# Performance work log

Hardware: AMD Instinct MI355X
Metric: run time of the kernel (lower is better)

Reference implementation:

```python
import jax, jax.numpy as jnp
import numpy as np

N = 524288          # total atoms (sorted by degree)
E = 1433600         # total directed bonds
B, L = 16384, 32    # molecules x atoms-per-molecule (B*L == N)
NODE, EDGE, H, OUT = 64, 16, 128, 128
N0 = 8192           # number of degree-0 atoms
DEG_COUNTS = {1: 65536, 2: 131072, 3: 196608, 4: 98304, 5: 24576}
BN_EPS = 1e-5


def setup_inputs() -> dict:
    key = jax.random.key(0)
    ks = jax.random.split(key, 24)
    inp = {}
    inp["node_feat"] = jax.random.normal(ks[0], (N, NODE), jnp.float32)
    inp["edge_feat"] = jax.random.normal(ks[1], (E, EDGE), jnp.float32)
    i = 2
    for d in (1, 2, 3, 4, 5):
        n_d = DEG_COUNTS[d]
        inp[f"nbr_node_d{d}"] = jax.random.randint(ks[i], (n_d, d), 0, N, jnp.int32); i += 1
        inp[f"nbr_edge_d{d}"] = jax.random.randint(ks[i], (n_d, d), 0, E, jnp.int32); i += 1
    inp["atom_index"] = jnp.arange(B * L, dtype=jnp.int32).reshape(B, L)

    def lin(k, o, fan_in):
        return jax.random.normal(k, (o, fan_in), jnp.float32) / np.sqrt(fan_in).astype(np.float32)

    inp["out_W0"] = lin(ks[12], OUT, NODE); inp["out_b0"] = jnp.zeros((OUT,), jnp.float32)
    inp["out_W1"] = lin(ks[13], OUT, H);    inp["out_b1"] = jnp.zeros((OUT,), jnp.float32)
    inp["out_W2"] = lin(ks[14], OUT, H);    inp["out_b2"] = jnp.zeros((OUT,), jnp.float32)
    inp["conv0_selfW"] = lin(ks[15], H, NODE)
    inp["conv0_degW"] = jax.random.normal(ks[16], (5, H, NODE + EDGE), jnp.float32) / np.sqrt(NODE + EDGE).astype(np.float32)
    inp["conv0_bias"] = jnp.zeros((1, H), jnp.float32)
    inp["conv1_selfW"] = lin(ks[17], H, H)
    inp["conv1_degW"] = jax.random.normal(ks[18], (5, H, H + EDGE), jnp.float32) / np.sqrt(H + EDGE).astype(np.float32)
    inp["conv1_bias"] = jnp.zeros((1, H), jnp.float32)
    return inp


def _graph_degree_conv(node_repr, edge_repr, selfW, degW, bias, nbr_nodes, nbr_edges):
    out_size = selfW.shape[0]
    # degree 0: zero neighbor contribution
    parts = [jnp.zeros((N0, out_size), node_repr.dtype)]
    for di, d in enumerate((1, 2, 3, 4, 5)):
        nn_rep = node_repr[nbr_nodes[di]]          # [n_d, d, node]
        ee_rep = edge_repr[nbr_edges[di]]          # [n_d, d, edge]
        summed = jnp.concatenate([nn_rep.sum(1), ee_rep.sum(1)], axis=-1)  # [n_d, node+edge]
        parts.append(summed @ degW[di].T)          # per-degree linear (no bias)
    neighbor_repr = jnp.concatenate(parts, axis=0)  # nodes sorted by degree -> aligned
    act = node_repr @ selfW.T + neighbor_repr + bias
    # BatchNorm1d(affine=False), training-mode batch stats (biased variance)
    mean = act.mean(0)
    var = act.var(0)
    act = (act - mean) / jnp.sqrt(var + BN_EPS)
    return jax.nn.relu(act)


def reference(node_feat, edge_feat,
              nbr_node_d1, nbr_edge_d1, nbr_node_d2, nbr_edge_d2,
              nbr_node_d3, nbr_edge_d3, nbr_node_d4, nbr_edge_d4,
              nbr_node_d5, nbr_edge_d5, atom_index,
              out_W0, out_b0, out_W1, out_b1, out_W2, out_b2,
              conv0_selfW, conv0_degW, conv0_bias,
              conv1_selfW, conv1_degW, conv1_bias):
    nbr_nodes = (nbr_node_d1, nbr_node_d2, nbr_node_d3, nbr_node_d4, nbr_node_d5)
    nbr_edges = (nbr_edge_d1, nbr_edge_d2, nbr_edge_d3, nbr_edge_d4, nbr_edge_d5)

    x = node_feat
    acc = jax.nn.softmax(x @ out_W0.T + out_b0, axis=1)
    x = _graph_degree_conv(x, edge_feat, conv0_selfW, conv0_degW, conv0_bias, nbr_nodes, nbr_edges)
    acc = acc + jax.nn.softmax(x @ out_W1.T + out_b1, axis=1)
    x = _graph_degree_conv(x, edge_feat, conv1_selfW, conv1_degW, conv1_bias, nbr_nodes, nbr_edges)
    acc = acc + jax.nn.softmax(x @ out_W2.T + out_b2, axis=1)
    # scatter per-atom activations into [batch, max_len, OUT]
    return acc[atom_index]
```

## Files before the change

kernel.cpp:

```cpp
#include <hip/hip_runtime.h>
#include <hip/hip_bf16.h>
#include <math.h>


typedef short  short8   __attribute__((ext_vector_type(8)));
typedef unsigned short ushort8v __attribute__((ext_vector_type(8)));
typedef float  f32x4    __attribute__((ext_vector_type(4)));
typedef unsigned int u32;

static constexpr int  N_ATOMS = 524288;
static constexpr long NROWCOL = (long)N_ATOMS * 128;
static constexpr int  NBLK    = N_ATOMS / 64;

__device__ __forceinline__ float bf2f(ushort h) {
    return __uint_as_float(((unsigned)h) << 16);
}
__device__ __forceinline__ ushort f2bf(float x) {
    unsigned u = __float_as_uint(x);
    return (ushort)((u + 0x7fffu + ((u >> 16) & 1u)) >> 16);
}

__device__ __forceinline__ uint4 pack8(const float v[8]) {
    union { __hip_bfloat162 h2[4]; uint4 u; } c;
#pragma unroll
    for (int e = 0; e < 4; ++e)
        c.h2[e] = __float22bfloat162_rn(make_float2(v[2*e], v[2*e+1]));
    return c.u;
}
__device__ __forceinline__ short8 pack8s(const float v[8]) {
    union { uint4 u; short8 s; } c;
    c.u = pack8(v);
    return c.s;
}
__device__ __forceinline__ ushort f2bf1(float x) {
    union { __hip_bfloat16 b; ushort u; } c;
    c.b = __float2bfloat16(x);
    return c.u;
}

__device__ __forceinline__ void gload_lds16(const ushort* g, ushort* l) {
    __builtin_amdgcn_global_load_lds(
        (const __attribute__((address_space(1))) u32*)g,
        (__attribute__((address_space(3))) u32*)l, 16, 0, 0);
}

__device__ __forceinline__ void seg_of(long r, int& d, long& off) {
    if      (r < 73728)  { d = 1; off = 8192;  }
    else if (r < 204800) { d = 2; off = 73728; }
    else if (r < 401408) { d = 3; off = 204800;}
    else if (r < 499712) { d = 4; off = 401408;}
    else                 { d = 5; off = 499712;}
}

__global__ __launch_bounds__(256)
void esum_kernel(const float* __restrict__ edge_feat,
                 const int* __restrict__ ne1, const int* __restrict__ ne2,
                 const int* __restrict__ ne3, const int* __restrict__ ne4,
                 const int* __restrict__ ne5, ushort* __restrict__ esumb)
{
    const long t = (long)blockIdx.x * 256 + threadIdx.x;
    const long r = 8192 + (t >> 1);
    const int  h = (int)(t & 1);
    int d; long off; seg_of(r, d, off);
    const int* ne = (d==1)?ne1:(d==2)?ne2:(d==3)?ne3:(d==4)?ne4:ne5;
    const long i0 = (r - off) * d;
    float v[8] = {0,0,0,0,0,0,0,0};
    for (int j = 0; j < d; ++j) {
        const long e = ne[i0 + j];
        const float4* p = (const float4*)(edge_feat + e * 16 + h * 8);
        const float4 a = p[0], b = p[1];
        v[0]+=a.x; v[1]+=a.y; v[2]+=a.z; v[3]+=a.w;
        v[4]+=b.x; v[5]+=b.y; v[6]+=b.z; v[7]+=b.w;
    }
    *(uint4*)(esumb + (r - 8192) * 16 + h * 8) = pack8(v);
}

__global__ void wprep(const float* __restrict__ src, ushort* __restrict__ dst,
                      int rows, int Ks, int Kd)
{
    const int i = blockIdx.x * 256 + threadIdx.x;
    if (i >= rows * Kd) return;
    const int r = i / Kd, c = i % Kd;
    dst[i] = f2bf(c < Ks ? src[r * Ks + c] : 0.f);
}

__global__ void wprep_img(const float* __restrict__ src, ushort* __restrict__ dst, int K)
{
    const int i = blockIdx.x * 256 + threadIdx.x;
    if (i >= 128 * K) return;
    const int row = i / K, col = i % K;
    dst[(col >> 3) * 1024 + row * 8 + (col & 7)] = f2bf(src[i]);
}

template<int NG, bool F32, bool BN>
__device__ __forceinline__ void stage_rows(const void* Xv, long r0,
                                           ushort* __restrict__ Ab,
                                           const float* __restrict__ statsL)
{
    for (int t = threadIdx.x; t < 64 * NG; t += 256) {
        const int row = t / NG, g = t % NG;
        const long gr = r0 + row;
        uint4 w;
        if (F32) {
            const float4* p = (const float4*)((const float*)Xv + gr * (long)(NG * 8) + g * 8);
            const float4 a = p[0], b = p[1];
            const float v[8] = {a.x,a.y,a.z,a.w,b.x,b.y,b.z,b.w};
            w = pack8(v);
        } else if (BN) {
            const int c0 = g * 8;
            const ushort8v u = *(const ushort8v*)((const ushort*)Xv + gr * (long)(NG * 8) + g * 8);
            float v[8];
#pragma unroll
            for (int e = 0; e < 8; ++e)
                v[e] = fmaxf(fmaf(bf2f(u[e]), statsL[c0 + e], statsL[128 + c0 + e]), 0.f);
            w = pack8(v);
        } else {
            w = *(const uint4*)((const ushort*)Xv + gr * (long)(NG * 8) + g * 8);
        }
        ((uint4*)Ab)[row * NG + (g ^ (row & 7))] = w;
    }
}

template<int NGL, int NST, int NGN, bool F32, bool BN>
__device__ __forceinline__ void stage_gather(const void* Xv,
                                             const ushort* __restrict__ esumb,
                                             const int* __restrict__ nnl, int d,
                                             long r0, ushort* __restrict__ Ab,
                                             const float* __restrict__ statsL)
{
    for (int t = threadIdx.x; t < 64 * NST; t += 256) {
        const int row = t / NST, g = t % NST;
        uint4 w = {0, 0, 0, 0};
        if (g < NGN) {
            const int c0 = g * 8;
            float v[8] = {0,0,0,0,0,0,0,0};
            for (int j = 0; j < d; ++j) {
                const long idx = nnl[row * d + j];
                if (F32) {
                    const float4* p = (const float4*)((const float*)Xv + idx * (long)(NGN * 8) + c0);
                    const float4 a = p[0], b = p[1];
                    v[0]+=a.x; v[1]+=a.y; v[2]+=a.z; v[3]+=a.w;
                    v[4]+=b.x; v[5]+=b.y; v[6]+=b.z; v[7]+=b.w;
                } else {
                    const ushort8v u = *(const ushort8v*)((const ushort*)Xv + idx * (long)(NGN * 8) + c0);
#pragma unroll
                    for (int e = 0; e < 8; ++e) {
                        float x = bf2f(u[e]);
                        if (BN) x = fmaxf(fmaf(x, statsL[c0 + e], statsL[128 + c0 + e]), 0.f);
                        v[e] += x;
                    }
                }
            }
            w = pack8(v);
        } else if (g < NGN + 2) {
            const long er = r0 + row - 8192;
            w = *(const uint4*)(esumb + er * 16 + (g - NGN) * 8);
        }
        ((uint4*)Ab)[row * NGL + (g ^ (row & 7))] = w;
    }
}

template<int KS, int NG>
__device__ __forceinline__ void mfma_lds(const ushort* __restrict__ Ab,
                                         const ushort* __restrict__ Wb, int KP,
                                         int wc, f32x4 acc[4][2])
{
    const int lane = threadIdx.x & 63;
    const int lg = lane >> 4, lr = lane & 15;
#pragma unroll
    for (int ks = 0; ks < KS; ++ks) {
        short8 B0 = *(const short8*)(Wb + (long)(wc + lr) * KP + ks * 32 + 8 * lg);
        short8 B1 = *(const short8*)(Wb + (long)(wc + 16 + lr) * KP + ks * 32 + 8 * lg);
        const int gk = ks * 4 + lg;
#pragma unroll
        for (int m = 0; m < 4; ++m) {
            const int row = 16 * m + lr;
            const short8 a = *(const short8*)(Ab + (row * NG + (gk ^ (row & 7))) * 8);
            acc[m][0] = __builtin_amdgcn_mfma_f32_16x16x32_bf16(a, B0, acc[m][0], 0, 0, 0);
            acc[m][1] = __builtin_amdgcn_mfma_f32_16x16x32_bf16(a, B1, acc[m][1], 0, 0, 0);
        }
    }
}

template<int K1, bool A1F32, bool BNIN, int NGL2, int NST2, int NGN2, int KS2, int KP2>
__global__ __launch_bounds__(256, 2)
void conv_kernel(const void* __restrict__ X, const ushort* __restrict__ Wb1,
                 const ushort* __restrict__ Wb2base,
                 const int* __restrict__ nn1, const int* __restrict__ nn2,
                 const int* __restrict__ nn3, const int* __restrict__ nn4,
                 const int* __restrict__ nn5,
                 const ushort* __restrict__ esumb, const float* __restrict__ cbias,
                 const float* __restrict__ stats_in,
                 ushort* __restrict__ act_out, float* __restrict__ part)
{
    constexpr int NG1 = K1 / 8;
    constexpr int KS1 = K1 / 32;
    constexpr int NGMAX = (NGL2 > NG1) ? NGL2 : NG1;
    __shared__ uint4 AbV[64 * NGMAX];
    __shared__ int   nnl[320];
    __shared__ float statsL[256];
    ushort* Ab = (ushort*)AbV;

    const long r0 = (long)blockIdx.x * 64;
    const int wid = threadIdx.x >> 6, lane = threadIdx.x & 63;
    const int lg = lane >> 4, lr = lane & 15, wc = wid * 32;

    if (BNIN)
        for (int t = threadIdx.x; t < 256; t += 256) statsL[t] = stats_in[t];

    int d = 0;
    const bool has2 = (r0 >= 8192);
    if (has2) {
        long off; seg_of(r0, d, off);
        const int* nn = (d==1)?nn1:(d==2)?nn2:(d==3)?nn3:(d==4)?nn4:nn5;
        const long i0 = (r0 - off) * d;
        for (int t = threadIdx.x; t < 64 * d; t += 256) nnl[t] = nn[i0 + t];
    }
    __syncthreads();

    stage_rows<NG1, A1F32, BNIN>(X, r0, Ab, statsL);
    __syncthreads();
    f32x4 acc[4][2] = {};
    mfma_lds<KS1, NG1>(Ab, Wb1, K1, wc, acc);

    if (has2) {
        __syncthreads();
        stage_gather<NGL2, NST2, NGN2, A1F32, BNIN>(X, esumb, nnl, d, r0, Ab, statsL);
        __syncthreads();
        const ushort* Wb2 = Wb2base + (long)(d - 1) * 128 * KP2;
        mfma_lds<KS2, NGL2>(Ab, Wb2, KP2, wc, acc);
    }

#pragma unroll
    for (int n = 0; n < 2; ++n) {
        const float bv = cbias[wc + n * 16 + lr];
#pragma unroll
        for (int m = 0; m < 4; ++m)
#pragma unroll
            for (int j = 0; j < 4; ++j) acc[m][n][j] += bv;
    }
#pragma unroll
    for (int m = 0; m < 4; ++m)
#pragma unroll
        for (int j = 0; j < 4; ++j) {
            const long row = r0 + 16 * m + 4 * lg + j;
#pragma unroll
            for (int n = 0; n < 2; ++n)
                act_out[row * 128 + wc + n * 16 + lr] = f2bf1(acc[m][n][j]);
        }
#pragma unroll
    for (int n = 0; n < 2; ++n) {
        float s = 0.f, q = 0.f;
#pragma unroll
        for (int m = 0; m < 4; ++m)
#pragma unroll
            for (int j = 0; j < 4; ++j) { const float v = acc[m][n][j]; s += v; q += v * v; }
        s += __shfl_xor(s, 16); s += __shfl_xor(s, 32);
        q += __shfl_xor(q, 16); q += __shfl_xor(q, 32);
        if (lane < 16) {
            part[(long)blockIdx.x * 256 + wc + n * 16 + lr]       = s;
            part[(long)blockIdx.x * 256 + 128 + wc + n * 16 + lr] = q;
        }
    }
}

__global__ __launch_bounds__(256)
void bn_finalize(const float* __restrict__ part, float* __restrict__ stats)
{
    const int c = blockIdx.x;
    float s = 0.f, q = 0.f;
    for (int b = threadIdx.x; b < NBLK; b += 256) {
        s += part[(long)b * 256 + c];
        q += part[(long)b * 256 + 128 + c];
    }
#pragma unroll
    for (int o = 1; o < 64; o <<= 1) { s += __shfl_xor(s, o); q += __shfl_xor(q, o); }
    __shared__ float rs[4], rq[4];
    const int wid = threadIdx.x >> 6;
    if ((threadIdx.x & 63) == 0) { rs[wid] = s; rq[wid] = q; }
    __syncthreads();
    if (threadIdx.x == 0) {
        s = rs[0] + rs[1] + rs[2] + rs[3];
        q = rq[0] + rq[1] + rq[2] + rq[3];
        const float mean = s * (1.0f / N_ATOMS);
        const float var  = q * (1.0f / N_ATOMS) - mean * mean;
        const float rstd = 1.0f / sqrtf(var + 1e-5f);
        stats[c]       = rstd;
        stats[128 + c] = -mean * rstd;
    }
}

__device__ __forceinline__ void mfma8_img(const ushort* __restrict__ Wl,
                                          int ks, int lg, int lr,
                                          short8 af, f32x4 (&acc)[8])
{
    const int a0 = (ks * 4 + lg) * 1024 + lr * 8;
#pragma unroll
    for (int n = 0; n < 8; ++n) {
        const short8 bf = *(const short8*)(Wl + a0 + n * 128);
        acc[n] = __builtin_amdgcn_mfma_f32_16x16x32_bf16(af, bf, acc[n], 0, 0, 0);
    }
}

__device__ __forceinline__ short8 cvt_bn(short8 u, int k0, const float* __restrict__ sl)
{
    float v[8];
#pragma unroll
    for (int e = 0; e < 8; ++e)
        v[e] = fmaxf(fmaf(bf2f((ushort)u[e]), sl[k0 + e], sl[128 + k0 + e]), 0.f);
    return pack8s(v);
}

__device__ __forceinline__ void softmax_accum(f32x4 (&acc)[8],
                                              const float* __restrict__ bias,
                                              int lr, f32x4 (&oacc)[8])
{
    float bb[8];
#pragma unroll
    for (int n = 0; n < 8; ++n) bb[n] = bias[n * 16 + lr];
#pragma unroll
    for (int j = 0; j < 4; ++j) {
        float s = 0.f;
#pragma unroll
        for (int n = 0; n < 8; ++n) {
            const float e = __expf(acc[n][j] + bb[n]);
            acc[n][j] = e; s += e;
        }
        s += __shfl_xor(s, 1); s += __shfl_xor(s, 2);
        s += __shfl_xor(s, 4); s += __shfl_xor(s, 8);
        const float inv = 1.0f / s;
#pragma unroll
        for (int n = 0; n < 8; ++n) oacc[n][j] += acc[n][j] * inv;
    }
}

__global__ __launch_bounds__(256, 4)
void out_kernel(const float* __restrict__ node, const ushort* __restrict__ act0b,
                const ushort* __restrict__ act1b, const ushort* __restrict__ wimg,
                const float* __restrict__ b0, const float* __restrict__ b1,
                const float* __restrict__ b2,
                const float* __restrict__ stats0, const float* __restrict__ stats1,
                float* __restrict__ out)
{
    __shared__ ushort Wlds[16384];
    __shared__ float sl[512];

    const int wid = threadIdx.x >> 6, lane = threadIdx.x & 63;
    const int lg = lane >> 4, lr = lane & 15;
    const long rA = (long)blockIdx.x * 64 + wid * 16 + lr;

#pragma unroll
    for (int i = 0; i < 8; ++i) {
        const int c = wid * 8 + i;
        gload_lds16(wimg + 8192 + c * 512 + lane * 8, &Wlds[c * 512]);
    }
    for (int t = threadIdx.x; t < 512; t += 256)
        sl[t] = (t < 256) ? stats0[t] : stats1[t - 256];

    short8 r1[4];
#pragma unroll
    for (int ks = 0; ks < 4; ++ks)
        r1[ks] = *(const short8*)(act0b + rA * 128 + ks * 32 + lg * 8);
    const float4* n0 = (const float4*)(node + rA * 64 + lg * 8);
    float4 h0a = n0[0], h0b = n0[1];

    __syncthreads();

    f32x4 oacc[8] = {};
    f32x4 acc[8] = {};
    {
#pragma unroll
        for (int ks = 0; ks < 4; ++ks)
            mfma8_img(Wlds, ks, lg, lr, cvt_bn(r1[ks], ks * 32 + lg * 8, sl), acc);
    }
    const float4* n1 = (const float4*)(node + rA * 64 + 32 + lg * 8);
    float4 h1a = n1[0], h1b = n1[1];
    short8 r2[4];
#pragma unroll
    for (int ks = 0; ks < 4; ++ks)
        r2[ks] = *(const short8*)(act1b + rA * 128 + ks * 32 + lg * 8);

    softmax_accum(acc, b1, lr, oacc);

    __syncthreads();
#pragma unroll
    for (int i = 0; i < 4; ++i) {
        const int c = wid * 4 + i;
        gload_lds16(wimg + c * 512 + lane * 8, &Wlds[c * 512]);
    }
    __syncthreads();

#pragma unroll
    for (int n = 0; n < 8; ++n) acc[n] = f32x4{0.f, 0.f, 0.f, 0.f};
    {
        const float v0[8] = {h0a.x,h0a.y,h0a.z,h0a.w,h0b.x,h0b.y,h0b.z,h0b.w};
        mfma8_img(Wlds, 0, lg, lr, pack8s(v0), acc);
        const float v1[8] = {h1a.x,h1a.y,h1a.z,h1a.w,h1b.x,h1b.y,h1b.z,h1b.w};
        mfma8_img(Wlds, 1, lg, lr, pack8s(v1), acc);
    }
    softmax_accum(acc, b0, lr, oacc);

    __syncthreads();
#pragma unroll
    for (int i = 0; i < 8; ++i) {
        const int c = wid * 8 + i;
        gload_lds16(wimg + 24576 + c * 512 + lane * 8, &Wlds[c * 512]);
    }
    __syncthreads();

#pragma unroll
    for (int n = 0; n < 8; ++n) acc[n] = f32x4{0.f, 0.f, 0.f, 0.f};
    {
#pragma unroll
        for (int ks = 0; ks < 4; ++ks)
            mfma8_img(Wlds, ks, lg, lr, cvt_bn(r2[ks], ks * 32 + lg * 8, sl + 256), acc);
    }
    softmax_accum(acc, b2, lr, oacc);

    const long rC0 = (long)blockIdx.x * 64 + wid * 16;
#pragma unroll
    for (int j = 0; j < 4; ++j) {
        const long row = rC0 + 4 * lg + j;
#pragma unroll
        for (int n = 0; n < 8; ++n)
            out[row * 128 + n * 16 + lr] = oacc[n][j];
    }
}

extern "C" void kernel_launch(void* const* d_in, const int* in_sizes, int n_in,
                              void* d_out, int out_size, void* d_ws, size_t ws_size,
                              hipStream_t stream)
{
    const float* node_feat = (const float*)d_in[0];
    const float* edge_feat = (const float*)d_in[1];
    const int* nn1 = (const int*)d_in[2];  const int* ne1 = (const int*)d_in[3];
    const int* nn2 = (const int*)d_in[4];  const int* ne2 = (const int*)d_in[5];
    const int* nn3 = (const int*)d_in[6];  const int* ne3 = (const int*)d_in[7];
    const int* nn4 = (const int*)d_in[8];  const int* ne4 = (const int*)d_in[9];
    const int* nn5 = (const int*)d_in[10]; const int* ne5 = (const int*)d_in[11];
    const float* W0     = (const float*)d_in[13];
    const float* b0     = (const float*)d_in[14];
    const float* W1     = (const float*)d_in[15];
    const float* b1     = (const float*)d_in[16];
    const float* W2     = (const float*)d_in[17];
    const float* b2     = (const float*)d_in[18];
    const float* selfW0 = (const float*)d_in[19];
    const float* degW0  = (const float*)d_in[20];
    const float* cb0    = (const float*)d_in[21];
    const float* selfW1 = (const float*)d_in[22];
    const float* degW1  = (const float*)d_in[23];
    const float* cb1    = (const float*)d_in[24];

    float*  part   = (float*)d_ws;
    float*  stats0 = part + (long)NBLK * 256;
    float*  stats1 = stats0 + 256;
    ushort* act0b  = (ushort*)(stats1 + 256);
    ushort* act1b  = act0b + NROWCOL;
    ushort* esumb  = act1b + NROWCOL;
    ushort* wb_self0 = esumb + (long)516096 * 16;
    ushort* wb_deg0  = wb_self0 + 128 * 64;
    ushort* wb_self1 = wb_deg0  + 640 * 96;
    ushort* wb_deg1  = wb_self1 + 128 * 128;
    ushort* wimg     = wb_deg1  + 640 * 160;
    const size_t needed = (size_t)((char*)(wimg + 40960) - (char*)d_ws);
    if (ws_size < needed) return;

    wprep<<<(128*64 +255)/256, 256, 0, stream>>>(selfW0, wb_self0, 128, 64, 64);
    wprep<<<(640*96 +255)/256, 256, 0, stream>>>(degW0,  wb_deg0,  640, 80, 96);
    wprep<<<(128*128+255)/256, 256, 0, stream>>>(selfW1, wb_self1, 128, 128, 128);
    wprep<<<(640*160+255)/256, 256, 0, stream>>>(degW1,  wb_deg1,  640, 144, 160);
    wprep_img<<<(128*64 +255)/256, 256, 0, stream>>>(W0, wimg,          64);
    wprep_img<<<(128*128+255)/256, 256, 0, stream>>>(W1, wimg + 8192,  128);
    wprep_img<<<(128*128+255)/256, 256, 0, stream>>>(W2, wimg + 24576, 128);

    esum_kernel<<<4032, 256, 0, stream>>>(edge_feat, ne1, ne2, ne3, ne4, ne5, esumb);

    conv_kernel<64, true, false, 16, 12, 8, 3, 96><<<NBLK, 256, 0, stream>>>(
        node_feat, wb_self0, wb_deg0, nn1, nn2, nn3, nn4, nn5, esumb, cb0,
        nullptr, act0b, part);
    bn_finalize<<<128, 256, 0, stream>>>(part, stats0);

    conv_kernel<128, false, true, 24, 20, 16, 5, 160><<<NBLK, 256, 0, stream>>>(
        act0b, wb_self1, wb_deg1, nn1, nn2, nn3, nn4, nn5, esumb, cb1,
        stats0, act1b, part);
    bn_finalize<<<128, 256, 0, stream>>>(part, stats1);

    out_kernel<<<NBLK, 256, 0, stream>>>(node_feat, act0b, act1b, wimg,
        b0, b1, b2, stats0, stats1, (float*)d_out);
}
```

Before: 574.5 us.

## Stage self rows and neighbor gather together in one LDS buffer

The LDS tile is enlarged to hold both the self-row operand and the gathered neighbor-plus-edge operand side by side. Both staging phases now run back to back before a single barrier, which removes two __syncthreads and lets the gather's global loads overlap with the self-row loads. The MFMA loop also preloads all weight fragments into registers before issuing MFMAs. The cost is more LDS per block and more VGPRs, which could limit occupancy.

```diff
diff --git a/kernel.cpp b/kernel.cpp
--- a/kernel.cpp
+++ b/kernel.cpp
@@ -92,7 +92,7 @@
     dst[(col >> 3) * 1024 + row * 8 + (col & 7)] = f2bf(src[i]);
 }
 
-template<int NG, bool F32, bool BN>
+template<int NGT, int NG, bool F32, bool BN>
 __device__ __forceinline__ void stage_rows(const void* Xv, long r0,
                                            ushort* __restrict__ Ab,
                                            const float* __restrict__ statsL)
@@ -117,17 +117,18 @@
         } else {
             w = *(const uint4*)((const ushort*)Xv + gr * (long)(NG * 8) + g * 8);
         }
-        ((uint4*)Ab)[row * NG + (g ^ (row & 7))] = w;
-    }
-}
-
-template<int NGL, int NST, int NGN, bool F32, bool BN>
+        ((uint4*)Ab)[row * NGT + (g ^ (row & 7))] = w;
+    }
+}
+
+template<int NGT, int GOFS, int NST, int NGN, bool F32, bool BN>
 __device__ __forceinline__ void stage_gather(const void* Xv,
                                              const ushort* __restrict__ esumb,
                                              const int* __restrict__ nnl, int d,
                                              long r0, ushort* __restrict__ Ab,
                                              const float* __restrict__ statsL)
 {
+    constexpr int KINW = (F32 ? NGN * 8 : 128);
     for (int t = threadIdx.x; t < 64 * NST; t += 256) {
         const int row = t / NST, g = t % NST;
         uint4 w = {0, 0, 0, 0};
@@ -137,12 +138,12 @@
             for (int j = 0; j < d; ++j) {
                 const long idx = nnl[row * d + j];
                 if (F32) {
-                    const float4* p = (const float4*)((const float*)Xv + idx * (long)(NGN * 8) + c0);
+                    const float4* p = (const float4*)((const float*)Xv + idx * (long)KINW + c0);
                     const float4 a = p[0], b = p[1];
                     v[0]+=a.x; v[1]+=a.y; v[2]+=a.z; v[3]+=a.w;
                     v[4]+=b.x; v[5]+=b.y; v[6]+=b.z; v[7]+=b.w;
                 } else {
-                    const ushort8v u = *(const ushort8v*)((const ushort*)Xv + idx * (long)(NGN * 8) + c0);
+                    const ushort8v u = *(const ushort8v*)((const ushort*)Xv + idx * (long)KINW + c0);
 #pragma unroll
                     for (int e = 0; e < 8; ++e) {
                         float x = bf2f(u[e]);
@@ -156,28 +157,32 @@
             const long er = r0 + row - 8192;
             w = *(const uint4*)(esumb + er * 16 + (g - NGN) * 8);
         }
-        ((uint4*)Ab)[row * NGL + (g ^ (row & 7))] = w;
-    }
-}
-
-template<int KS, int NG>
-__device__ __forceinline__ void mfma_lds(const ushort* __restrict__ Ab,
-                                         const ushort* __restrict__ Wb, int KP,
-                                         int wc, f32x4 acc[4][2])
+        ((uint4*)Ab)[row * NGT + GOFS + (g ^ (row & 7))] = w;
+    }
+}
+
+template<int KS, int NGT, int GOFS>
+__device__ __forceinline__ void mfma_phase(const ushort* __restrict__ Ab,
+                                           const ushort* __restrict__ Wb, int KP,
+                                           int wc, f32x4 acc[4][2])
 {
     const int lane = threadIdx.x & 63;
     const int lg = lane >> 4, lr = lane & 15;
+    short8 B[KS][2];
 #pragma unroll
     for (int ks = 0; ks < KS; ++ks) {
-        short8 B0 = *(const short8*)(Wb + (long)(wc + lr) * KP + ks * 32 + 8 * lg);
-        short8 B1 = *(const short8*)(Wb + (long)(wc + 16 + lr) * KP + ks * 32 + 8 * lg);
+        B[ks][0] = *(const short8*)(Wb + (long)(wc + lr) * KP + ks * 32 + 8 * lg);
+        B[ks][1] = *(const short8*)(Wb + (long)(wc + 16 + lr) * KP + ks * 32 + 8 * lg);
+    }
+#pragma unroll
+    for (int ks = 0; ks < KS; ++ks) {
         const int gk = ks * 4 + lg;
 #pragma unroll
         for (int m = 0; m < 4; ++m) {
             const int row = 16 * m + lr;
-            const short8 a = *(const short8*)(Ab + (row * NG + (gk ^ (row & 7))) * 8);
-            acc[m][0] = __builtin_amdgcn_mfma_f32_16x16x32_bf16(a, B0, acc[m][0], 0, 0, 0);
-            acc[m][1] = __builtin_amdgcn_mfma_f32_16x16x32_bf16(a, B1, acc[m][1], 0, 0, 0);
+            const short8 a = *(const short8*)(Ab + (row * NGT + GOFS + (gk ^ (row & 7))) * 8);
+            acc[m][0] = __builtin_amdgcn_mfma_f32_16x16x32_bf16(a, B[ks][0], acc[m][0], 0, 0, 0);
+            acc[m][1] = __builtin_amdgcn_mfma_f32_16x16x32_bf16(a, B[ks][1], acc[m][1], 0, 0, 0);
         }
     }
 }
@@ -195,8 +200,8 @@
 {
     constexpr int NG1 = K1 / 8;
     constexpr int KS1 = K1 / 32;
-    constexpr int NGMAX = (NGL2 > NG1) ? NGL2 : NG1;
-    __shared__ uint4 AbV[64 * NGMAX];
+    constexpr int NGT = NG1 + NGL2;
+    __shared__ uint4 AbV[64 * NGT];
     __shared__ int   nnl[320];
     __shared__ float statsL[256];
     ushort* Ab = (ushort*)AbV;
@@ -218,17 +223,16 @@
     }
     __syncthreads();
 
-    stage_rows<NG1, A1F32, BNIN>(X, r0, Ab, statsL);
-    __syncthreads();
+    stage_rows<NGT, NG1, A1F32, BNIN>(X, r0, Ab, statsL);
+    if (has2)
+        stage_gather<NGT, NG1, NST2, NGN2, A1F32, BNIN>(X, esumb, nnl, d, r0, Ab, statsL);
+    __syncthreads();
+
     f32x4 acc[4][2] = {};
-    mfma_lds<KS1, NG1>(Ab, Wb1, K1, wc, acc);
-
+    mfma_phase<KS1, NGT, 0>(Ab, Wb1, K1, wc, acc);
     if (has2) {
-        __syncthreads();
-        stage_gather<NGL2, NST2, NGN2, A1F32, BNIN>(X, esumb, nnl, d, r0, Ab, statsL);
-        __syncthreads();
         const ushort* Wb2 = Wb2base + (long)(d - 1) * 128 * KP2;
-        mfma_lds<KS2, NGL2>(Ab, Wb2, KP2, wc, acc);
+        mfma_phase<KS2, NGT, NG1>(Ab, Wb2, KP2, wc, acc);
     }
 
 #pragma unroll
```

Measured after the change: 619.0 us. 1.08x slower.
